# Kernel tuning notes

Measured on AMD Instinct MI355X. Metric: run time of the kernel, lower is better.

## Reference

```python
import jax, jax.numpy as jnp
import numpy as np

B, N, D = 4, 2048, 1024
H, DH = 16, 64
MAX_POS_EMB = 256
TOPK = 64


def setup_inputs() -> dict:
    key = jax.random.key(0)
    ks = jax.random.split(key, 8)
    s = 0.02
    inner = H * DH
    return {
        "x": jax.random.normal(ks[0], (B, N, D), jnp.float32),
        "gating_mask": jax.random.uniform(ks[1], (B, 1, N, 1), jnp.float32),
        "Wq": jax.random.normal(ks[2], (D, inner), jnp.float32) * s,
        "bq": jnp.zeros((inner,), jnp.float32),
        "Wkv": jax.random.normal(ks[3], (D, 2 * inner), jnp.float32) * s,
        "bkv": jnp.zeros((2 * inner,), jnp.float32),
        "Wo": jax.random.normal(ks[4], (inner, D), jnp.float32) * s,
        "bo": jnp.zeros((D,), jnp.float32),
        "rel_emb": jax.random.normal(ks[5], (MAX_POS_EMB, DH), jnp.float32) * s,
        "mask": jnp.ones((B, N), bool),
        "sparse_topk": TOPK,
    }


def reference(x, gating_mask, Wq, bq, Wkv, bkv, Wo, bo, rel_emb, mask, sparse_topk):
    b, n, d = x.shape
    h, dh = H, DH
    scale = dh ** -0.5
    mask_val = -jnp.finfo(x.dtype).max

    # projections -> [b, h, n, dh]
    q = (x @ Wq + bq).reshape(b, n, h, dh).transpose(0, 2, 1, 3)
    kv = x @ Wkv + bkv
    k = kv[..., : h * dh].reshape(b, n, h, dh).transpose(0, 2, 1, 3)
    v = kv[..., h * dh:].reshape(b, n, h, dh).transpose(0, 2, 1, 3)

    dots = jnp.einsum("bhid,bhjd->bhij", q, k) * scale  # [b,h,n,n]

    # relative positional bias: q . E[clip(i-j+M, 0, M-1)]
    seq = jnp.arange(n)
    dist = jnp.clip(seq[:, None] - seq[None, :] + MAX_POS_EMB, 0, MAX_POS_EMB - 1)
    qE = jnp.einsum("bhid,rd->bhir", q, rel_emb) * scale  # [b,h,n,R]
    pos_attn = jnp.take_along_axis(qE, dist[None, None, :, :], axis=-1)  # [b,h,n,n]
    dots = dots + pos_attn

    # padding mask: mask_i * mask_j
    full_mask = mask[:, None, :, None] & mask[:, None, None, :]
    dots = jnp.where(full_mask, dots, mask_val)

    # topk sparsification: keep only scores >= k-th largest per row
    top = jax.lax.top_k(dots, sparse_topk)[0]  # [b,h,n,topk]
    vk = top[..., -1:]
    dots = jnp.where(dots < vk, mask_val, dots)

    attn = jax.nn.softmax(dots, axis=-1)
    attn = attn * gating_mask

    out = jnp.einsum("bhij,bhjd->bhid", attn, v)
    out = out.transpose(0, 2, 1, 3).reshape(b, n, h * dh)
    return out @ Wo + bo
```

## Files before the change

### kernel.cpp

```cpp
#include <hip/hip_runtime.h>
#include <stdint.h>


typedef __attribute__((ext_vector_type(8))) short short8;
typedef __attribute__((ext_vector_type(4))) float floatx4;
typedef _Float16 f16x2 __attribute__((ext_vector_type(2)));

#define Bn   4
#define Nn   2048
#define Hn   16
#define BHn  (Bn*Hn)
#define DELTA 0.0025f

__device__ __forceinline__ float bf2f(unsigned short u) {
  union { unsigned int i; float f; } v; v.i = ((unsigned int)u) << 16; return v.f;
}
__device__ __forceinline__ unsigned short f2bf(float f) {
  union { float f; unsigned int i; } v; v.f = f;
  unsigned int r = v.i + 0x7fffu + ((v.i >> 16) & 1u);
  return (unsigned short)(r >> 16);
}
__device__ __forceinline__ floatx4 mfma16(short8 a, short8 b, floatx4 c) {
  return __builtin_amdgcn_mfma_f32_16x16x32_bf16(a, b, c, 0, 0, 0);
}
__device__ __forceinline__ void split2(float x, unsigned short& h, unsigned short& m) {
  h = f2bf(x);
  m = f2bf(x - bf2f(h));
}
__device__ __forceinline__ void split3(float x, unsigned short& h, unsigned short& m, unsigned short& l) {
  h = f2bf(x);
  float r = x - bf2f(h);
  m = f2bf(r);
  l = f2bf(r - bf2f(m));
}
__device__ __forceinline__ unsigned int mapf(float f) {
  union { _Float16 h; unsigned short s; } u; u.h = (_Float16)f;
  unsigned int b = (unsigned int)u.s;
  return (b & 0x8000u) ? (b ^ 0xFFFFu) : (b | 0x8000u);
}
__device__ __forceinline__ float unmapf(unsigned int c) {
  unsigned int b = (c & 0x8000u) ? (c ^ 0x8000u) : (c ^ 0xFFFFu);
  union { _Float16 h; unsigned short s; } u; u.s = (unsigned short)b;
  return (float)u.h;
}

__global__ __launch_bounds__(256)
void transpose_split3(const float* __restrict__ W,
                      unsigned short* __restrict__ T0,
                      unsigned short* __restrict__ T1,
                      unsigned short* __restrict__ T2,
                      int K, int Ncols)
{
  __shared__ float tile[32][33];
  int k0 = blockIdx.y * 32, n0 = blockIdx.x * 32;
  int tx = threadIdx.x & 31, ty = threadIdx.x >> 5;
  for (int s = 0; s < 32; s += 8)
    tile[ty + s][tx] = W[(size_t)(k0 + ty + s) * Ncols + n0 + tx];
  __syncthreads();
  for (int s = 0; s < 32; s += 8) {
    float x = tile[tx][ty + s];
    unsigned short h, m, l;
    split3(x, h, m, l);
    size_t o = (size_t)(n0 + ty + s) * K + k0 + tx;
    T0[o] = h; T1[o] = m; T2[o] = l;
  }
}

__global__ __launch_bounds__(256)
void transpose_split2(const float* __restrict__ W,
                      unsigned short* __restrict__ T0,
                      unsigned short* __restrict__ T1,
                      int K, int Ncols)
{
  __shared__ float tile[32][33];
  int k0 = blockIdx.y * 32, n0 = blockIdx.x * 32;
  int tx = threadIdx.x & 31, ty = threadIdx.x >> 5;
  for (int s = 0; s < 32; s += 8)
    tile[ty + s][tx] = W[(size_t)(k0 + ty + s) * Ncols + n0 + tx];
  __syncthreads();
  for (int s = 0; s < 32; s += 8) {
    float x = tile[tx][ty + s];
    unsigned short h, m;
    split2(x, h, m);
    size_t o = (size_t)(n0 + ty + s) * K + k0 + tx;
    T0[o] = h; T1[o] = m;
  }
}

__global__ __launch_bounds__(256)
void convert_bf16(const float* __restrict__ in, unsigned short* __restrict__ outp, int n) {
  int i = blockIdx.x * 256 + threadIdx.x;
  if (i < n) outp[i] = f2bf(in[i]);
}

__global__ __launch_bounds__(256)
void gemm_qkv(const float* __restrict__ A,
              const unsigned short* __restrict__ B0,
              const unsigned short* __restrict__ B1,
              const unsigned short* __restrict__ B2,
              const float* __restrict__ bias,
              float* __restrict__ O32,
              unsigned short* __restrict__ Oh,
              unsigned short* __restrict__ Om,
              _Float16* __restrict__ Vh,
              int K, float scale)
{
  __shared__ unsigned short lA[3][128 * 40];
  __shared__ unsigned short lB[3][128 * 40];
  const int tid = threadIdx.x;
  const int lane = tid & 63;
  const int m0 = blockIdx.y * 128, n0 = blockIdx.x * 128;
  const bool vblk = (n0 >= 1024);
  const int wid = tid >> 6, wm = wid >> 1, wn = wid & 1;
  const int fr = lane & 15, fq = lane >> 4;
  floatx4 acc[4][4] = {};

  for (int k0 = 0; k0 < K; k0 += 32) {
    __syncthreads();
    #pragma unroll
    for (int p = 0; p < 2; p++) {
      int c = tid + p * 256;
      int row = c >> 2, kc = (c & 3) * 8;
      size_t go = (size_t)(m0 + row) * K + k0 + kc;
      float4 v0 = *(const float4*)&A[go];
      float4 v1 = *(const float4*)&A[go + 4];
      union { unsigned short u[8]; uint4 q; } hh, mm, ll;
      float xs[8] = {v0.x, v0.y, v0.z, v0.w, v1.x, v1.y, v1.z, v1.w};
      #pragma unroll
      for (int e = 0; e < 8; e++) split3(xs[e], hh.u[e], mm.u[e], ll.u[e]);
      *(uint4*)&lA[0][row * 40 + kc] = hh.q;
      *(uint4*)&lA[1][row * 40 + kc] = mm.q;
      size_t bo = (size_t)(n0 + row) * K + k0 + kc;
      *(uint4*)&lB[0][row * 40 + kc] = *(const uint4*)&B0[bo];
      *(uint4*)&lB[1][row * 40 + kc] = *(const uint4*)&B1[bo];
      if (!vblk) {
        *(uint4*)&lA[2][row * 40 + kc] = ll.q;
        *(uint4*)&lB[2][row * 40 + kc] = *(const uint4*)&B2[bo];
      }
    }
    __syncthreads();
    short8 af0[4], af1[4], af2[4], bf0[4], bf1[4], bf2v[4];
    #pragma unroll
    for (int t = 0; t < 4; t++) {
      int ao = (wm * 64 + t * 16 + fr) * 40 + 8 * fq;
      int bo2 = (wn * 64 + t * 16 + fr) * 40 + 8 * fq;
      af0[t] = *(const short8*)&lA[0][ao];
      af1[t] = *(const short8*)&lA[1][ao];
      bf0[t] = *(const short8*)&lB[0][bo2];
      bf1[t] = *(const short8*)&lB[1][bo2];
      if (!vblk) {
        af2[t] = *(const short8*)&lA[2][ao];
        bf2v[t] = *(const short8*)&lB[2][bo2];
      }
    }
    #pragma unroll
    for (int mi = 0; mi < 4; mi++)
      #pragma unroll
      for (int ni = 0; ni < 4; ni++) {
        acc[mi][ni] = mfma16(af0[mi], bf0[ni], acc[mi][ni]);
        acc[mi][ni] = mfma16(af0[mi], bf1[ni], acc[mi][ni]);
        acc[mi][ni] = mfma16(af1[mi], bf0[ni], acc[mi][ni]);
        if (!vblk) {
          acc[mi][ni] = mfma16(af1[mi], bf1[ni], acc[mi][ni]);
          acc[mi][ni] = mfma16(af0[mi], bf2v[ni], acc[mi][ni]);
          acc[mi][ni] = mfma16(af2[mi], bf0[ni], acc[mi][ni]);
        }
      }
  }
  #pragma unroll
  for (int mi = 0; mi < 4; mi++)
    #pragma unroll
    for (int ni = 0; ni < 4; ni++) {
      int nl = n0 + wn * 64 + ni * 16 + fr;
      float bv = bias[nl];
      #pragma unroll
      for (int rg = 0; rg < 4; rg++) {
        int ml = m0 + wm * 64 + mi * 16 + fq * 4 + rg;
        float val = (acc[mi][ni][rg] + bv) * scale;
        int bb = ml >> 11, ii = ml & 2047;
        int hh2 = (nl & 1023) >> 6, dd = nl & 63;
        size_t idx = (((size_t)bb * Hn + hh2) * Nn + ii) * 64 + dd;
        if (!vblk) {
          O32[idx] = val;
          unsigned short h, m;
          split2(val, h, m);
          Oh[idx] = h; Om[idx] = m;
        } else {
          Vh[idx] = (_Float16)val;
        }
      }
    }
}

__global__ __launch_bounds__(256)
void gemm_out(const float* __restrict__ A,
              const unsigned short* __restrict__ B0,
              const unsigned short* __restrict__ B1,
              const float* __restrict__ bias,
              float* __restrict__ O32,
              int Ncols, int K)
{
  __shared__ unsigned short lA[2][128 * 40];
  __shared__ unsigned short lB[2][128 * 40];
  const int tid = threadIdx.x;
  const int lane = tid & 63;
  const int m0 = blockIdx.y * 128, n0 = blockIdx.x * 128;
  const int wid = tid >> 6, wm = wid >> 1, wn = wid & 1;
  const int fr = lane & 15, fq = lane >> 4;
  floatx4 acc[4][4] = {};

  for (int k0 = 0; k0 < K; k0 += 32) {
    __syncthreads();
    #pragma unroll
    for (int p = 0; p < 2; p++) {
      int c = tid + p * 256;
      int row = c >> 2, kc = (c & 3) * 8;
      size_t go = (size_t)(m0 + row) * K + k0 + kc;
      float4 v0 = *(const float4*)&A[go];
      float4 v1 = *(const float4*)&A[go + 4];
      union { unsigned short u[8]; uint4 q; } hh, mm;
      float xs[8] = {v0.x, v0.y, v0.z, v0.w, v1.x, v1.y, v1.z, v1.w};
      #pragma unroll
      for (int e = 0; e < 8; e++) split2(xs[e], hh.u[e], mm.u[e]);
      *(uint4*)&lA[0][row * 40 + kc] = hh.q;
      *(uint4*)&lA[1][row * 40 + kc] = mm.q;
      size_t bo = (size_t)(n0 + row) * K + k0 + kc;
      *(uint4*)&lB[0][row * 40 + kc] = *(const uint4*)&B0[bo];
      *(uint4*)&lB[1][row * 40 + kc] = *(const uint4*)&B1[bo];
    }
    __syncthreads();
    short8 af[2][4], bfr[2][4];
    #pragma unroll
    for (int s = 0; s < 2; s++)
      #pragma unroll
      for (int t = 0; t < 4; t++) {
        af[s][t]  = *(const short8*)&lA[s][(wm * 64 + t * 16 + fr) * 40 + 8 * fq];
        bfr[s][t] = *(const short8*)&lB[s][(wn * 64 + t * 16 + fr) * 40 + 8 * fq];
      }
    #pragma unroll
    for (int mi = 0; mi < 4; mi++)
      #pragma unroll
      for (int ni = 0; ni < 4; ni++) {
        acc[mi][ni] = mfma16(af[0][mi], bfr[0][ni], acc[mi][ni]);
        acc[mi][ni] = mfma16(af[0][mi], bfr[1][ni], acc[mi][ni]);
        acc[mi][ni] = mfma16(af[1][mi], bfr[0][ni], acc[mi][ni]);
      }
  }
  #pragma unroll
  for (int mi = 0; mi < 4; mi++)
    #pragma unroll
    for (int ni = 0; ni < 4; ni++) {
      int nl = n0 + wn * 64 + ni * 16 + fr;
      float bv = bias[nl];
      #pragma unroll
      for (int rg = 0; rg < 4; rg++) {
        int ml = m0 + wm * 64 + mi * 16 + fq * 4 + rg;
        O32[(size_t)ml * Ncols + nl] = acc[mi][ni][rg] + bv;
      }
    }
}

__global__ __launch_bounds__(1024, 8)
void attn_k(const unsigned short* __restrict__ qh,
            const unsigned short* __restrict__ qm,
            const unsigned short* __restrict__ kh,
            const unsigned short* __restrict__ km,
            const _Float16* __restrict__ vh,
            const float* __restrict__ q32,
            const float* __restrict__ k32,
            const unsigned short* __restrict__ relbf,
            const float* __restrict__ rel32,
            const float* __restrict__ gating,
            const int* __restrict__ topkp,
            float* __restrict__ inner)
{
  extern __shared__ char smem[];
  _Float16* S = (_Float16*)smem;
  unsigned short* KtH = (unsigned short*)(smem + 65536);
  unsigned short* KtM = KtH + 4096;
  _Float16* qE = (_Float16*)KtH;

  const int wgid = blockIdx.x;
  const int xcd = wgid & 7;
  const int idx = wgid >> 3;
  const int bh = xcd * 8 + (idx >> 7);
  const int ib = idx & 127;
  const int i0 = ib * 16;
  const int b = bh >> 4, h = bh & 15;
  const int tid = threadIdx.x;
  const int lane = tid & 63, w = tid >> 6;
  const int fr = lane & 15, fq = lane >> 4;
  const int topk = topkp[0];

  const size_t qoff = ((size_t)bh * Nn + i0) * 64;
  const size_t qf = qoff + (size_t)fr * 64 + 8 * fq;
  const short8 aqh0 = *(const short8*)&qh[qf];
  const short8 aqh1 = *(const short8*)&qh[qf + 32];
  const short8 aqm0 = *(const short8*)&qm[qf];
  const short8 aqm1 = *(const short8*)&qm[qf + 32];

  {
    const int sel = tid >> 9;
    const int row = (tid >> 3) & 63, ch = tid & 7;
    const int dst = row * 64 + ((ch ^ (row & 7)) * 8);
    unsigned short* T = sel ? KtM : KtH;
    const unsigned short* src = sel ? km : kh;
    const size_t gbase = (size_t)bh * Nn * 64 + (size_t)row * 64 + ch * 8;
    uint4 rr = *(const uint4*)&src[gbase];

    for (int jt = 0; jt < 32; jt++) {
      __syncthreads();
      *(uint4*)&T[dst] = rr;
      if (jt + 1 < 32)
        rr = *(const uint4*)&src[gbase + (size_t)(jt + 1) * 4096];
      __syncthreads();
      if (w < 8 && ((jt & 1) == (w >> 2))) {
        int wc = w & 3;
        int row16 = wc * 16 + fr, r7 = fr & 7;
        int b0 = row16 * 64 + ((fq ^ r7) * 8);
        int b1 = row16 * 64 + (((fq + 4) ^ r7) * 8);
        __builtin_amdgcn_s_setprio(1);
        floatx4 c = {};
        {
          short8 kh0 = *(const short8*)&KtH[b0];
          short8 kh1 = *(const short8*)&KtH[b1];
          c = mfma16(aqh0, kh0, c);
          c = mfma16(aqm0, kh0, c);
          c = mfma16(aqh1, kh1, c);
          c = mfma16(aqm1, kh1, c);
        }
        {
          short8 km0 = *(const short8*)&KtM[b0];
          short8 km1 = *(const short8*)&KtM[b1];
          c = mfma16(aqh0, km0, c);
          c = mfma16(aqh1, km1, c);
        }
        __builtin_amdgcn_s_setprio(0);
        int colsw = jt * 64 + ((wc ^ fq) * 16) + fr;
        #pragma unroll
        for (int rg = 0; rg < 4; rg++)
          S[(fq * 4 + rg) * 2048 + colsw] = (_Float16)c[rg];
      }
    }
  }
  __syncthreads();

  {
    size_t rf = (size_t)(w * 16 + fr) * 64 + 8 * fq;
    short8 rb0 = *(const short8*)&relbf[rf];
    short8 rb1 = *(const short8*)&relbf[rf + 32];
    floatx4 c = {};
    c = mfma16(aqh0, rb0, c); c = mfma16(aqh1, rb1, c);
    c = mfma16(aqm0, rb0, c); c = mfma16(aqm1, rb1, c);
    int colsw = ((w ^ fq) * 16) + fr;
    #pragma unroll
    for (int rg = 0; rg < 4; rg++)
      qE[(fq * 4 + rg) * 256 + colsw] = (_Float16)c[rg];
  }
  __syncthreads();

  const int r = w;
  const int i = i0 + r;
  const int X = (r >> 2) << 4;
  _Float16* S0 = S + r * 2048;
  const _Float16* qE0 = qE + r * 256;
  union pun { unsigned int u; f16x2 h; };
  pun cAp, cCp;
  cAp.h[0] = qE0[255 ^ X]; cAp.h[1] = cAp.h[0];
  cCp.h[0] = qE0[X];       cCp.h[1] = cCp.h[0];
  const int swl = (2 * lane) ^ X;

  unsigned int kk[16];
  unsigned int mh = 0, ml = 0;
  #pragma unroll
  for (int e = 0; e < 16; e++) {
    const int jb = 128 * e;
    pun sv, ev;
    sv.u = *(const unsigned int*)&S0[jb + swl];
    if (jb + 127 <= i) ev = cAp;
    else if (jb >= i + 256) ev = cCp;
    else {
      const int j0 = jb + 2 * lane;
      int c0 = i - j0 + 256; c0 = c0 < 0 ? 0 : (c0 > 255 ? 255 : c0);
      int c1 = i - j0 + 255; c1 = c1 < 0 ? 0 : (c1 > 255 ? 255 : c1);
      ev.h[0] = qE0[c0 ^ X]; ev.h[1] = qE0[c1 ^ X];
    }
    pun rv; rv.h = sv.h + ev.h;
    unsigned int u = rv.u;
    unsigned int sgn = (u >> 15) & 0x00010001u;
    unsigned int code = u ^ (sgn * 0x7FFFu + 0x80008000u);
    kk[e] = code;
    unsigned int chi = code & 0xFFFF0000u, clo = code << 16;
    mh = mh > chi ? mh : chi;
    ml = ml > clo ? ml : clo;
  }
  unsigned int umax = (mh > ml ? mh : ml) >> 16;
  unsigned int mxu = umax, mnu = umax;
  #pragma unroll
  for (int d = 1; d < 64; d <<= 1) {
    unsigned int o1 = (unsigned int)__shfl_xor((int)mxu, d);
    unsigned int o2 = (unsigned int)__shfl_xor((int)mnu, d);
    mxu = o1 > mxu ? o1 : mxu;
    mnu = o2 < mnu ? o2 : mnu;
  }
  const float mxv = unmapf(mxu);

  unsigned int lo = mnu, hi = mxu + 1;
  #pragma unroll 1
  for (int it = 0; it < 13; it++) {
    unsigned int mid = (lo + hi) >> 1;
    int cnt = 0;
    #pragma unroll
    for (int e = 0; e < 16; e++) {
      cnt += (int)__popcll(__ballot((kk[e] >> 16) >= mid));
      cnt += (int)__popcll(__ballot((kk[e] & 0xffffu) >= mid));
    }
    if (cnt >= topk) lo = mid; else hi = mid;
  }
  const float Cv = unmapf(hi) + 2.0f * DELTA;
  const float Lv = unmapf(lo) - 2.0f * DELTA;
  const unsigned int Cu = mapf(Cv) + 1;
  int Lsi = (int)mapf(Lv) - 1;
  const unsigned int Lu = Lsi < 0 ? 0u : (unsigned int)Lsi;

  char* sb = (char*)S0;
  unsigned int* Pk = (unsigned int*)sb;
  int*   Jc = (int*)(sb + 512);
  float* Sx = (float*)(sb + 768);
  float* P2 = (float*)(sb + 1024);
  asm volatile("" ::: "memory");
  const unsigned long long lmlt = (1ull << lane) - 1ull;

  int base = 0, mc = 0;
  #pragma unroll
  for (int t = 0; t < 32; t++) {
    unsigned int code = (t & 1) ? (kk[t >> 1] >> 16) : (kk[t >> 1] & 0xffffu);
    const int j = 2 * lane + 128 * (t >> 1) + (t & 1);
    bool dk = code >= Cu;
    bool cd = (code >= Lu) && !dk;
    unsigned long long mk = __ballot(dk);
    if (dk) { int pos = base + __popcll(mk & lmlt); Pk[pos] = (unsigned int)j | (code << 16); }
    base += __popcll(mk);
    mk = __ballot(cd);
    if (cd) { int pos = mc + __popcll(mk & lmlt); if (pos < 64) Jc[pos] = j; }
    mc += __popcll(mk);
  }
  if (mc > 64) mc = 64;
  asm volatile("" ::: "memory");

  const double qv = (double)q32[((size_t)bh * Nn + i) * 64 + lane];
  #pragma unroll 1
  for (int c2 = 0; c2 < mc; c2++) {
    int j = Jc[c2];
    int ridx = i - j + 256; ridx = ridx < 0 ? 0 : (ridx > 255 ? 255 : ridx);
    double t2 = qv * ((double)k32[((size_t)bh * Nn + j) * 64 + lane] +
                      (double)rel32[ridx * 64 + lane]);
    #pragma unroll
    for (int d = 1; d < 64; d <<= 1) t2 += __shfl_xor(t2, d);
    if (lane == 0) Sx[c2] = (float)t2;
  }
  asm volatile("" ::: "memory");

  const int need = topk - base;
  float myx = (lane < mc) ? Sx[lane] : -3.0e38f;
  int rank = 0;
  #pragma unroll 1
  for (int c2 = 0; c2 < mc; c2++) {
    float o = Sx[c2];
    rank += (o > myx || (o == myx && c2 < lane)) ? 1 : 0;
  }
  unsigned long long bm = __ballot((lane < mc) && (rank == need - 1));
  float vk = bm ? __shfl(myx, (int)__ffsll(bm) - 1) : 3.0e38f;
  bool ck = (lane < mc) && ((rank < need) || (myx == vk));
  unsigned long long km2 = __ballot(ck);
  float pb = 0.f;
  if (ck) {
    int pos = base + __popcll(km2 & lmlt);
    Pk[pos] = (unsigned int)Jc[lane];
    pb = __expf(myx - mxv);
    P2[pos] = pb;
  }
  const int nk = base + __popcll(km2);
  float ps = pb;
  #pragma unroll 1
  for (int t = lane; t < base; t += 64) {
    float val = unmapf(Pk[t] >> 16);
    float p = __expf(val - mxv);
    P2[t] = p; ps += p;
  }
  #pragma unroll
  for (int d = 1; d < 64; d <<= 1) ps += __shfl_xor(ps, d);
  const float coef = gating[(size_t)b * Nn + i] / ps;
  asm volatile("" ::: "memory");

  const _Float16* vbp = vh + (size_t)bh * Nn * 64 + lane;
  float a0 = 0.f, a1 = 0.f, a2 = 0.f, a3 = 0.f;
  int t4 = nk & ~3;
  #pragma unroll 1
  for (int t = 0; t < t4; t += 4) {
    int j0 = (int)(Pk[t] & 0xffffu), j1 = (int)(Pk[t + 1] & 0xffffu);
    int j2 = (int)(Pk[t + 2] & 0xffffu), j3 = (int)(Pk[t + 3] & 0xffffu);
    float p0 = P2[t], p1 = P2[t + 1], p2 = P2[t + 2], p3 = P2[t + 3];
    a0 += p0 * (float)vbp[(size_t)j0 * 64];
    a1 += p1 * (float)vbp[(size_t)j1 * 64];
    a2 += p2 * (float)vbp[(size_t)j2 * 64];
    a3 += p3 * (float)vbp[(size_t)j3 * 64];
  }
  #pragma unroll 1
  for (int t = t4; t < nk; t++)
    a0 += P2[t] * (float)vbp[(size_t)(Pk[t] & 0xffffu) * 64];
  inner[((size_t)b * Nn + i) * 1024 + h * 64 + lane] = (a0 + a1 + a2 + a3) * coef;
}

extern "C" void kernel_launch(void* const* d_in, const int* in_sizes, int n_in,
                              void* d_out, int out_size, void* d_ws, size_t ws_size,
                              hipStream_t stream) {
  const float* x      = (const float*)d_in[0];
  const float* gating = (const float*)d_in[1];
  const float* Wq     = (const float*)d_in[2];
  const float* bq     = (const float*)d_in[3];
  const float* Wkv    = (const float*)d_in[4];
  const float* bkv    = (const float*)d_in[5];
  const float* Wo     = (const float*)d_in[6];
  const float* bo     = (const float*)d_in[7];
  const float* rel    = (const float*)d_in[8];
  const int*   topk   = (const int*)d_in[10];
  float* out = (float*)d_out;

  char* ws = (char*)d_ws;
  size_t off = 0;
  auto alloc = [&](size_t bytes) -> void* {
    void* p = ws + off; off += (bytes + 255) & ~(size_t)255; return p;
  };
  unsigned short* Wqt0 = (unsigned short*)alloc(1024ull * 1024 * 2);
  unsigned short* Wqt1 = (unsigned short*)alloc(1024ull * 1024 * 2);
  unsigned short* Wqt2 = (unsigned short*)alloc(1024ull * 1024 * 2);
  unsigned short* Wkt0 = (unsigned short*)alloc(2048ull * 1024 * 2);
  unsigned short* Wkt1 = (unsigned short*)alloc(2048ull * 1024 * 2);
  unsigned short* Wkt2 = (unsigned short*)alloc(2048ull * 1024 * 2);
  unsigned short* Wot0 = (unsigned short*)alloc(1024ull * 1024 * 2);
  unsigned short* Wot1 = (unsigned short*)alloc(1024ull * 1024 * 2);
  unsigned short* relbf = (unsigned short*)alloc(256ull * 64 * 2);
  float* q32 = (float*)alloc((size_t)BHn * Nn * 64 * 4);
  float* k32 = (float*)alloc((size_t)BHn * Nn * 64 * 4);
  unsigned short* qhb = (unsigned short*)alloc((size_t)BHn * Nn * 64 * 2);
  unsigned short* qmb = (unsigned short*)alloc((size_t)BHn * Nn * 64 * 2);
  unsigned short* khb = (unsigned short*)alloc((size_t)BHn * Nn * 64 * 2);
  unsigned short* kmb = (unsigned short*)alloc((size_t)BHn * Nn * 64 * 2);
  _Float16* vhb = (_Float16*)alloc((size_t)BHn * Nn * 64 * 2);
  float* inner = (float*)alloc((size_t)Bn * Nn * 1024 * 4);
  if (off > ws_size) return;

  size_t shmem = 65536 + 16384;
  (void)hipFuncSetAttribute((const void*)attn_k,
                            hipFuncAttributeMaxDynamicSharedMemorySize, (int)shmem);

  transpose_split3<<<dim3(32, 32), 256, 0, stream>>>(Wq, Wqt0, Wqt1, Wqt2, 1024, 1024);
  transpose_split3<<<dim3(64, 32), 256, 0, stream>>>(Wkv, Wkt0, Wkt1, Wkt2, 1024, 2048);
  transpose_split2<<<dim3(32, 32), 256, 0, stream>>>(Wo, Wot0, Wot1, 1024, 1024);
  convert_bf16<<<dim3(64), 256, 0, stream>>>(rel, relbf, 256 * 64);

  gemm_qkv<<<dim3(8, 64), 256, 0, stream>>>(x, Wqt0, Wqt1, Wqt2, bq,
      q32, qhb, qmb, vhb, 1024, 0.125f);
  gemm_qkv<<<dim3(16, 64), 256, 0, stream>>>(x, Wkt0, Wkt1, Wkt2, bkv,
      k32, khb, kmb, vhb, 1024, 1.0f);

  attn_k<<<dim3(8192), 1024, shmem, stream>>>(qhb, qmb, khb, kmb, vhb,
      q32, k32, relbf, rel, gating, topk, inner);

  gemm_out<<<dim3(8, 64), 256, 0, stream>>>(inner, Wot0, Wot1, bo,
      out, 1024, 1024);
}
```

Measured before the change: 1.117 ms.

## Double-buffer kh staging in LDS, read km from global, fix PV loop bound

```diff
diff --git a/kernel.cpp b/kernel.cpp
--- a/kernel.cpp
+++ b/kernel.cpp
@@ -276,9 +276,9 @@
 {
   extern __shared__ char smem[];
   _Float16* S = (_Float16*)smem;
-  unsigned short* KtH = (unsigned short*)(smem + 65536);
-  unsigned short* KtM = KtH + 4096;
-  _Float16* qE = (_Float16*)KtH;
+  unsigned short* Kt0 = (unsigned short*)(smem + 65536);
+  unsigned short* Kt1 = Kt0 + 4096;
+  _Float16* qE = (_Float16*)Kt0;
 
   const int wgid = blockIdx.x;
   const int xcd = wgid & 7;
@@ -291,6 +291,7 @@
   const int lane = tid & 63, w = tid >> 6;
   const int fr = lane & 15, fq = lane >> 4;
   const int topk = topkp[0];
+  const size_t kbase = (size_t)bh * Nn * 64;
 
   const size_t qoff = ((size_t)bh * Nn + i0) * 64;
   const size_t qf = qoff + (size_t)fr * 64 + 8 * fq;
@@ -300,50 +301,53 @@
   const short8 aqm1 = *(const short8*)&qm[qf + 32];
 
   {
-    const int sel = tid >> 9;
-    const int row = (tid >> 3) & 63, ch = tid & 7;
-    const int dst = row * 64 + ((ch ^ (row & 7)) * 8);
-    unsigned short* T = sel ? KtM : KtH;
-    const unsigned short* src = sel ? km : kh;
-    const size_t gbase = (size_t)bh * Nn * 64 + (size_t)row * 64 + ch * 8;
-    uint4 rr = *(const uint4*)&src[gbase];
+    const bool stager = (tid >= 512);
+    const int sidx = tid & 511;
+    const int srow = sidx >> 3, sch = sidx & 7;
+    const int sdst = srow * 64 + ((sch ^ (srow & 7)) * 8);
+    const size_t sgbase = kbase + (size_t)srow * 64 + sch * 8;
+    uint4 rr = {};
+    if (stager) {
+      rr = *(const uint4*)&kh[sgbase];
+      *(uint4*)&Kt0[sdst] = rr;
+      rr = *(const uint4*)&kh[sgbase + 4096];
+    }
+    __syncthreads();
 
     for (int jt = 0; jt < 32; jt++) {
-      __syncthreads();
-      *(uint4*)&T[dst] = rr;
-      if (jt + 1 < 32)
-        rr = *(const uint4*)&src[gbase + (size_t)(jt + 1) * 4096];
-      __syncthreads();
-      if (w < 8 && ((jt & 1) == (w >> 2))) {
+      if (stager) {
+        unsigned short* Kn = (jt & 1) ? Kt0 : Kt1;
+        if (jt + 1 < 32) *(uint4*)&Kn[sdst] = rr;
+        if (jt + 2 < 32)
+          rr = *(const uint4*)&kh[sgbase + (size_t)(jt + 2) * 4096];
+      } else if ((jt & 1) == (w >> 2)) {
+        const unsigned short* Kc = (jt & 1) ? Kt1 : Kt0;
         int wc = w & 3;
         int row16 = wc * 16 + fr, r7 = fr & 7;
         int b0 = row16 * 64 + ((fq ^ r7) * 8);
         int b1 = row16 * 64 + (((fq + 4) ^ r7) * 8);
+        const size_t kf = kbase + (size_t)(jt * 64 + row16) * 64 + 8 * fq;
         __builtin_amdgcn_s_setprio(1);
         floatx4 c = {};
-        {
-          short8 kh0 = *(const short8*)&KtH[b0];
-          short8 kh1 = *(const short8*)&KtH[b1];
-          c = mfma16(aqh0, kh0, c);
-          c = mfma16(aqm0, kh0, c);
-          c = mfma16(aqh1, kh1, c);
-          c = mfma16(aqm1, kh1, c);
-        }
-        {
-          short8 km0 = *(const short8*)&KtM[b0];
-          short8 km1 = *(const short8*)&KtM[b1];
-          c = mfma16(aqh0, km0, c);
-          c = mfma16(aqh1, km1, c);
-        }
+        short8 m0 = *(const short8*)&km[kf];
+        short8 m1 = *(const short8*)&km[kf + 32];
+        short8 h0 = *(const short8*)&Kc[b0];
+        short8 h1 = *(const short8*)&Kc[b1];
+        c = mfma16(aqh0, h0, c);
+        c = mfma16(aqm0, h0, c);
+        c = mfma16(aqh1, h1, c);
+        c = mfma16(aqm1, h1, c);
+        c = mfma16(aqh0, m0, c);
+        c = mfma16(aqh1, m1, c);
         __builtin_amdgcn_s_setprio(0);
         int colsw = jt * 64 + ((wc ^ fq) * 16) + fr;
         #pragma unroll
         for (int rg = 0; rg < 4; rg++)
           S[(fq * 4 + rg) * 2048 + colsw] = (_Float16)c[rg];
       }
-    }
-  }
-  __syncthreads();
+      __syncthreads();
+    }
+  }
 
   {
     size_t rf = (size_t)(w * 16 + fr) * 64 + 8 * fq;
@@ -495,9 +499,8 @@
 
   const _Float16* vbp = vh + (size_t)bh * Nn * 64 + lane;
   float a0 = 0.f, a1 = 0.f, a2 = 0.f, a3 = 0.f;
-  int t4 = nk & ~3;
   #pragma unroll 1
-  for (int t = 0; t < t4; t += 4) {
+  for (int t = 0; t < 64; t += 4) {
     int j0 = (int)(Pk[t] & 0xffffu), j1 = (int)(Pk[t + 1] & 0xffffu);
     int j2 = (int)(Pk[t + 2] & 0xffffu), j3 = (int)(Pk[t + 3] & 0xffffu);
     float p0 = P2[t], p1 = P2[t + 1], p2 = P2[t + 2], p3 = P2[t + 3];
@@ -507,7 +510,7 @@
     a3 += p3 * (float)vbp[(size_t)j3 * 64];
   }
   #pragma unroll 1
-  for (int t = t4; t < nk; t++)
+  for (int t = 64; t < nk; t++)
     a0 += P2[t] * (float)vbp[(size_t)(Pk[t] & 0xffffu) * 64];
   inner[((size_t)b * Nn + i) * 1024 + h * 64 + lane] = (a0 + a1 + a2 + a3) * coef;
 }
```

Result: slower. 1.236 ms (+10.6%).
